# Optimization experiments

Hardware: AMD Instinct MI355X
Metric: run time of the kernel (lower is better)

## Reference

```python
import jax, jax.numpy as jnp
import numpy as np
from jax import lax

B, T = 16384, 10
H = 256
CAR_V, REG_V, POI_V, WEEK_V, TIME_V = 1000000, 100000, 1000, 7, 1440
LABELS = 500
IN = 39  # 16+8+4+3+8


def _lstm_layer(x, Wih, Whh, bih, bhh):
    # x: [B, T, D] -> outputs [B, T, H]; PyTorch gate order i,f,g,o
    b = x.shape[0]
    h0 = jnp.zeros((b, H), x.dtype)
    c0 = jnp.zeros((b, H), x.dtype)
    # Precompute input projections for all timesteps in one GEMM
    xg = jnp.einsum('btd,gd->btg', x, Wih) + bih + bhh  # [B, T, 4H]

    def step(carry, xt_g):
        h, c = carry
        gates = xt_g + h @ Whh.T  # [B, 4H]
        i, f, g, o = jnp.split(gates, 4, axis=-1)
        i, f, o = jax.nn.sigmoid(i), jax.nn.sigmoid(f), jax.nn.sigmoid(o)
        g = jnp.tanh(g)
        c = f * c + i * g
        h = o * jnp.tanh(c)
        return (h, c), h

    _, ys = lax.scan(step, (h0, c0), xg.transpose(1, 0, 2))  # ys: [T, B, H]
    return ys.transpose(1, 0, 2)


def setup_inputs() -> dict:
    key = jax.random.key(0)
    ks = jax.random.split(key, 20)
    s = 0.05
    return {
        'car_idx': jax.random.randint(ks[0], (B, T), 0, CAR_V),
        'region_idx': jax.random.randint(ks[1], (B, T), 0, REG_V),
        'poi_idx': jax.random.randint(ks[2], (B, T), 0, POI_V),
        'week_idx': jax.random.randint(ks[3], (B, T), 0, WEEK_V),
        'time_idx': jax.random.randint(ks[4], (B, T), 0, TIME_V),
        'car_emb': jax.random.normal(ks[5], (CAR_V, 16), jnp.float32) * s,
        'region_emb': jax.random.normal(ks[6], (REG_V, 8), jnp.float32) * s,
        'poi_emb': jax.random.normal(ks[7], (POI_V, 4), jnp.float32) * s,
        'week_emb': jax.random.normal(ks[8], (WEEK_V, 3), jnp.float32) * s,
        'time_emb': jax.random.normal(ks[9], (TIME_V, 8), jnp.float32) * s,
        'Wih0': jax.random.normal(ks[10], (4 * H, IN), jnp.float32) * s,
        'Whh0': jax.random.normal(ks[11], (4 * H, H), jnp.float32) * s,
        'bih0': jax.random.normal(ks[12], (4 * H,), jnp.float32) * s,
        'bhh0': jax.random.normal(ks[13], (4 * H,), jnp.float32) * s,
        'Wih1': jax.random.normal(ks[14], (4 * H, H), jnp.float32) * s,
        'Whh1': jax.random.normal(ks[15], (4 * H, H), jnp.float32) * s,
        'bih1': jax.random.normal(ks[16], (4 * H,), jnp.float32) * s,
        'bhh1': jax.random.normal(ks[17], (4 * H,), jnp.float32) * s,
        'Wout': jax.random.normal(ks[18], (LABELS, H), jnp.float32) * s,
        'bout': jax.random.normal(ks[19], (LABELS,), jnp.float32) * s,
    }


def reference(car_idx, region_idx, poi_idx, week_idx, time_idx,
              car_emb, region_emb, poi_emb, week_emb, time_emb,
              Wih0, Whh0, bih0, bhh0, Wih1, Whh1, bih1, bhh1,
              Wout, bout):
    # Batched version of the original per-item embedding-lookup + concat loop
    x = jnp.concatenate([
        car_emb[car_idx],      # [B, T, 16]
        region_emb[region_idx],  # [B, T, 8]
        poi_emb[poi_idx],      # [B, T, 4]
        week_emb[week_idx],    # [B, T, 3]
        time_emb[time_idx],    # [B, T, 8]
    ], axis=-1)  # [B, T, 39]
    h1 = _lstm_layer(x, Wih0, Whh0, bih0, bhh0)
    h2 = _lstm_layer(h1, Wih1, Whh1, bih1, bhh1)
    return h2[:, -1, :] @ Wout.T + bout  # [B, LABELS]
```

## Files before the change

### kernel.cpp

```cpp
#include <hip/hip_runtime.h>
#include <hip/hip_bf16.h>

#define BB 16384
#define TT 10
#define NLAB 500

typedef __attribute__((ext_vector_type(8))) __bf16 bf16x8;
typedef __attribute__((ext_vector_type(4))) float f32x4;
typedef __attribute__((ext_vector_type(8))) short short8v;

__device__ __forceinline__ unsigned short f2bf(float f) {
  union { float f; unsigned int u; } x; x.f = f;
  unsigned int r = 0x7fffu + ((x.u >> 16) & 1u);
  return (unsigned short)((x.u + r) >> 16);
}

__device__ __forceinline__ float sigm(float x) {
  return __builtin_amdgcn_rcpf(1.f + __builtin_amdgcn_exp2f(-1.4426950408889634f * x));
}
__device__ __forceinline__ float tanh_(float x) {
  float e = __builtin_amdgcn_exp2f(-2.8853900817779268f * x);
  return 2.f * __builtin_amdgcn_rcpf(1.f + e) - 1.f;
}

__device__ __forceinline__ void gload_lds16(const unsigned short* g, unsigned short* l) {
  __builtin_amdgcn_global_load_lds(
      (const __attribute__((address_space(1))) unsigned int*)g,
      (__attribute__((address_space(3))) unsigned int*)l, 16, 0, 0);
}

#define SCHED0() __builtin_amdgcn_sched_barrier(0)
#define BAR_LGKM()                                                       \
  { SCHED0(); asm volatile("s_waitcnt lgkmcnt(0)" ::: "memory");         \
    __builtin_amdgcn_s_barrier(); SCHED0(); }
#define BAR_LGKM_VM4()                                                   \
  { SCHED0(); asm volatile("s_waitcnt vmcnt(4) lgkmcnt(0)" ::: "memory");\
    __builtin_amdgcn_s_barrier(); SCHED0(); }

__global__ void prep_w(const float* __restrict__ Wih0, const float* __restrict__ Whh0,
                       const float* __restrict__ bih0, const float* __restrict__ bhh0,
                       const float* __restrict__ Wih1, const float* __restrict__ Whh1,
                       const float* __restrict__ bih1, const float* __restrict__ bhh1,
                       const float* __restrict__ Wout, const float* __restrict__ bout,
                       unsigned short* __restrict__ wall, float* __restrict__ bblob) {
  int i = blockIdx.x * 256 + threadIdx.x;
  if (i < 983040) {
    int c = i >> 14, r = i & 16383;
    int wid = r >> 11, frag = (r >> 9) & 3, lane = (r >> 3) & 63, e = r & 7;
    int kin = ((lane >> 4) << 3) + e;
    float v;
    if (c < 20) {
      int pass = c / 10, ks = c % 10;
      int n = (pass * 2 + (frag >> 1)) * 256 + wid * 32 + (frag & 1) * 16 + (lane & 15);
      int k = ks * 32 + kin;
      if (k < 64) v = (k < 39) ? Wih0[n * 39 + k] : 0.f;
      else        v = Whh0[n * 256 + (k - 64)];
    } else if (c < 52) {
      int idx = c - 20;
      int pass = idx >> 4, half = (idx >> 3) & 1, ks = idx & 7;
      int n = (pass * 2 + (frag >> 1)) * 256 + wid * 32 + (frag & 1) * 16 + (lane & 15);
      int k = ks * 32 + kin;
      v = half ? Wih1[n * 256 + k]
               : Whh1[n * 256 + k];
    } else {
      int ks = c - 52;
      int n = wid * 64 + frag * 16 + (lane & 15);
      int k = ks * 32 + kin;
      v = (n < NLAB) ? Wout[n * 256 + k] : 0.f;
    }
    wall[i] = f2bf(v);
  } else {
    int j = i - 983040;
    if (j < 1024)       bblob[j] = bih0[j] + bhh0[j];
    else if (j < 2048)  bblob[j] = bih1[j - 1024] + bhh1[j - 1024];
    else if (j < 2560) { int n = j - 2048; bblob[j] = (n < NLAB) ? bout[n] : 0.f; }
  }
}

__global__ void gather_x(const int* __restrict__ car_idx, const int* __restrict__ region_idx,
                         const int* __restrict__ poi_idx, const int* __restrict__ week_idx,
                         const int* __restrict__ time_idx,
                         const float* __restrict__ car_emb, const float* __restrict__ region_emb,
                         const float* __restrict__ poi_emb, const float* __restrict__ week_emb,
                         const float* __restrict__ time_emb,
                         unsigned short* __restrict__ xfrag) {
  int tid = blockIdx.x * 256 + threadIdx.x;
  if (tid >= BB * TT) return;
  int t = tid / BB;
  int b = tid - t * BB;
  int ii = b * TT + t;
  float v[64];
#pragma unroll
  for (int k = 0; k < 64; ++k) v[k] = 0.f;
  { const float* p = car_emb + (size_t)car_idx[ii] * 16;
#pragma unroll
    for (int k = 0; k < 16; ++k) v[k] = p[k]; }
  { const float* p = region_emb + (size_t)region_idx[ii] * 8;
#pragma unroll
    for (int k = 0; k < 8; ++k) v[16 + k] = p[k]; }
  { const float* p = poi_emb + (size_t)poi_idx[ii] * 4;
#pragma unroll
    for (int k = 0; k < 4; ++k) v[24 + k] = p[k]; }
  { const float* p = week_emb + (size_t)week_idx[ii] * 3;
#pragma unroll
    for (int k = 0; k < 3; ++k) v[28 + k] = p[k]; }
  { const float* p = time_emb + (size_t)time_idx[ii] * 8;
#pragma unroll
    for (int k = 0; k < 8; ++k) v[31 + k] = p[k]; }

  int tile = b >> 6, rb = (b >> 4) & 3, lrow = b & 15;
  size_t base = ((size_t)tile * TT + t) * 4096;
#pragma unroll
  for (int c = 0; c < 8; ++c) {
    int kc = c >> 2;
    int lane = lrow + ((c & 3) << 4);
    size_t off = base + (size_t)((((kc << 2) + rb) << 6) + lane) * 8;
    short8v s;
#pragma unroll
    for (int e = 0; e < 8; ++e) s[e] = (short)f2bf(v[c * 8 + e]);
    *(short8v*)(xfrag + off) = s;
  }
}

__device__ __forceinline__ f32x4 MF(bf16x8 a, bf16x8 b, f32x4 c) {
  return __builtin_amdgcn_mfma_f32_16x16x32_bf16(a, b, c, 0, 0, 0);
}

template <int NKS, int SPLIT>
__device__ __forceinline__ void gemm_pass(f32x4 (&acc)[2][2][4], bf16x8 (&bc)[4],
    const unsigned short* wpBase, const unsigned short* wnextFirst,
    const unsigned short* ab1, const unsigned short* ab2, int R0, int lane) {
#define AADDR(J) \
  ((SPLIT < NKS && (J) >= SPLIT) ? (ab2 + ((J) - SPLIT) * 2048) : (ab1 + (J) * 2048))
#define MFMA16(AREG, BREG)                                              \
  { __builtin_amdgcn_s_setprio(1);                                     \
    _Pragma("unroll")                                                   \
    for (int gl = 0; gl < 2; ++gl)                                      \
      _Pragma("unroll")                                                 \
      for (int nb = 0; nb < 2; ++nb)                                    \
        _Pragma("unroll")                                               \
        for (int rb = 0; rb < 4; ++rb)                                  \
          acc[gl][nb][rb] = MF(AREG[rb], BREG[gl * 2 + nb], acc[gl][nb][rb]); \
    __builtin_amdgcn_s_setprio(0); }

  int j = R0;
  bf16x8 aA[4], aB[4];
  {
    const unsigned short* ap = AADDR(j);
#pragma unroll
    for (int rb = 0; rb < 4; ++rb) aA[rb] = *(const bf16x8*)(ap + rb * 512 + lane * 8);
  }
#pragma unroll 1
  for (int i = 0; i < NKS; i += 2) {
    int j1 = j + 1; if (j1 == NKS) j1 = 0;
    bf16x8 bn[4];
    const unsigned short* w1 = wpBase + (size_t)j1 * 16384;
#pragma unroll
    for (int f = 0; f < 4; ++f) bn[f] = *(const bf16x8*)(w1 + f * 512);
    const unsigned short* an = AADDR(j1);
#pragma unroll
    for (int rb = 0; rb < 4; ++rb) aB[rb] = *(const bf16x8*)(an + rb * 512 + lane * 8);
    MFMA16(aA, bc)
    int j2 = j1 + 1; if (j2 == NKS) j2 = 0;
    const unsigned short* w2 = (i + 2 < NKS) ? (wpBase + (size_t)j2 * 16384) : wnextFirst;
#pragma unroll
    for (int f = 0; f < 4; ++f) bc[f] = *(const bf16x8*)(w2 + f * 512);
    const unsigned short* an2 = AADDR((i + 2 < NKS) ? j2 : j1);
#pragma unroll
    for (int rb = 0; rb < 4; ++rb) aA[rb] = *(const bf16x8*)(an2 + rb * 512 + lane * 8);
    MFMA16(aB, bn)
    j = j2;
  }
#undef MFMA16
#undef AADDR
}

__device__ __forceinline__ void partial_if(f32x4 (&acc)[2][2][4], f32x4 (&cst)[2][4],
                                           float* sib) {
#pragma unroll
  for (int nb = 0; nb < 2; ++nb)
#pragma unroll
    for (int rb = 0; rb < 4; ++rb)
#pragma unroll
      for (int r = 0; r < 4; ++r) {
        sib[((nb << 4) + (rb << 2) + r) << 6] = sigm(acc[0][nb][rb][r]);
        cst[nb][rb][r] = sigm(acc[1][nb][rb][r]) * cst[nb][rb][r];
      }
}

__device__ __forceinline__ void finish_go(f32x4 (&acc)[2][2][4], f32x4 (&cst)[2][4],
    const float* sib, unsigned short* hbuf, int lane, int wid) {
  int lrow = ((lane >> 4) << 2);
  int l15 = lane & 15;
#pragma unroll
  for (int nb = 0; nb < 2; ++nb) {
    int jw = (nb << 4) + l15;
    int lane_dst_base = ((jw >> 3) << 4);
    int elem = jw & 7;
#pragma unroll
    for (int rb = 0; rb < 4; ++rb)
#pragma unroll
      for (int r = 0; r < 4; ++r) {
        float g = tanh_(acc[0][nb][rb][r]);
        float o = sigm(acc[1][nb][rb][r]);
        float c = cst[nb][rb][r] + sib[((nb << 4) + (rb << 2) + r) << 6] * g;
        cst[nb][rb][r] = c;
        float h = o * tanh_(c);
        int lane_dst = lrow + r + lane_dst_base;
        hbuf[(size_t)((((wid << 2) + rb) << 6) + lane_dst) * 8 + elem] = f2bf(h);
      }
  }
}

__global__ __launch_bounds__(512, 1) void lstm_fused(
    const unsigned short* __restrict__ xfrag, const unsigned short* __restrict__ wall,
    const float* __restrict__ bblob, float* __restrict__ out) {
  __shared__ __align__(16) unsigned short h1s[16384];
  __shared__ __align__(16) unsigned short h2s[16384];
  __shared__ __align__(16) unsigned short xts[4096];
  __shared__ __align__(16) float bls[2560];
  __shared__ __align__(16) float sis[16384];

  int tid = threadIdx.x, lane = tid & 63, wid = tid >> 6;
  int tile = blockIdx.x, b0 = tile << 6, l15 = lane & 15;

  int R = (tile >> 3) & 15;
  int r2 = R & 1, r8 = R & 7, r16 = R;
  int r10 = (R < 10) ? R : (R - 10);

  for (int i = tid; i < 2560; i += 512) bls[i] = bblob[i];
  gload_lds16(xfrag + (size_t)(tile * TT) * 4096 + wid * 512 + lane * 8, xts + wid * 512);

  float* sib = sis + (wid << 11) + lane;

  const unsigned short* wb = wall + wid * 2048 + lane * 8;

  bf16x8 bc[4];
  {
    const unsigned short* b0p = wb + (size_t)r2 * 16384;
#pragma unroll
    for (int f = 0; f < 4; ++f) bc[f] = *(const bf16x8*)(b0p + f * 512);
  }

  asm volatile("s_waitcnt vmcnt(0)" ::: "memory");
  __syncthreads();

  f32x4 c1[2][4], c2[2][4];
#pragma unroll
  for (int nb = 0; nb < 2; ++nb)
#pragma unroll
    for (int rb = 0; rb < 4; ++rb) {
      c1[nb][rb] = (f32x4){0.f, 0.f, 0.f, 0.f};
      c2[nb][rb] = (f32x4){0.f, 0.f, 0.f, 0.f};
    }
  f32x4 acc[2][2][4];

#define ACC_BIAS(BOFF, GBASE)                                                     \
  _Pragma("unroll")                                                               \
  for (int gl = 0; gl < 2; ++gl)                                                  \
    _Pragma("unroll")                                                             \
    for (int nb = 0; nb < 2; ++nb) {                                              \
      float bv = bls[(BOFF) + (((GBASE) + gl) << 8) + (wid << 5) + (nb << 4) + l15]; \
      _Pragma("unroll")                                                           \
      for (int rb = 0; rb < 4; ++rb) acc[gl][nb][rb] = (f32x4){bv, bv, bv, bv};   \
    }

  ACC_BIAS(0, 0)
  gemm_pass<2, 2>(acc, bc, wb, wb + 163840 + (size_t)r2 * 16384, xts, xts, r2, lane);
  partial_if(acc, c1, sib);
  ACC_BIAS(0, 2)
  gemm_pass<2, 2>(acc, bc, wb + 163840, wb + 458752 + (size_t)r8 * 16384, xts, xts, r2, lane);
  BAR_LGKM()
  gload_lds16(xfrag + (size_t)(tile * TT + 1) * 4096 + wid * 512 + lane * 8,
              xts + wid * 512);
  finish_go(acc, c1, sib, h1s, lane, wid);
  ACC_BIAS(1024, 0)
  BAR_LGKM()
  gemm_pass<8, 8>(acc, bc, wb + 458752, wb + 720896 + (size_t)r8 * 16384, h1s, h1s, r8, lane);
  partial_if(acc, c2, sib);
  ACC_BIAS(1024, 2)
  gemm_pass<8, 8>(acc, bc, wb + 720896, wb + (size_t)r10 * 16384, h1s, h1s, r8, lane);
  BAR_LGKM_VM4()
  finish_go(acc, c2, sib, h2s, lane, wid);

#pragma unroll 1
  for (int t = 1; t < TT; ++t) {
    ACC_BIAS(0, 0)
    gemm_pass<10, 2>(acc, bc, wb, wb + 163840 + (size_t)r10 * 16384, xts, h1s, r10, lane);
    partial_if(acc, c1, sib);
    ACC_BIAS(0, 2)
    gemm_pass<10, 2>(acc, bc, wb + 163840, wb + 327680 + (size_t)r8 * 16384, xts, h1s, r10, lane);
    BAR_LGKM()
    if (t < TT - 1)
      gload_lds16(xfrag + (size_t)(tile * TT + t + 1) * 4096 + wid * 512 + lane * 8,
                  xts + wid * 512);
    finish_go(acc, c1, sib, h1s, lane, wid);
    ACC_BIAS(1024, 0)
    gemm_pass<8, 8>(acc, bc, wb + 327680, wb + 458752 + (size_t)r8 * 16384, h2s, h2s, r8, lane);
    BAR_LGKM()
    gemm_pass<8, 8>(acc, bc, wb + 458752, wb + 589824 + (size_t)r16 * 16384, h1s, h1s, r8, lane);
    partial_if(acc, c2, sib);
    ACC_BIAS(1024, 2)
    gemm_pass<16, 8>(acc, bc, wb + 589824,
                     (t < TT - 1) ? (wb + (size_t)r10 * 16384)
                                  : (wb + 851968 + (size_t)r8 * 16384),
                     h2s, h1s, r16, lane);
    BAR_LGKM_VM4()
    finish_go(acc, c2, sib, h2s, lane, wid);
  }
  BAR_LGKM()

#pragma unroll
  for (int gl = 0; gl < 2; ++gl)
#pragma unroll
    for (int nb = 0; nb < 2; ++nb) {
      float bv = bls[2048 + (wid << 6) + ((gl * 2 + nb) << 4) + l15];
#pragma unroll
      for (int rb = 0; rb < 4; ++rb) acc[gl][nb][rb] = (f32x4){bv, bv, bv, bv};
    }
  gemm_pass<8, 8>(acc, bc, wb + 851968, wb + 851968, h2s, h2s, r8, lane);

#pragma unroll
  for (int gl = 0; gl < 2; ++gl)
#pragma unroll
    for (int nb = 0; nb < 2; ++nb) {
      int n = (wid << 6) + ((gl * 2 + nb) << 4) + l15;
      if (n < NLAB) {
#pragma unroll
        for (int rb = 0; rb < 4; ++rb)
#pragma unroll
          for (int r = 0; r < 4; ++r) {
            int row = (rb << 4) + ((lane >> 4) << 2) + r;
            out[(size_t)(b0 + row) * NLAB + n] = acc[gl][nb][rb][r];
          }
      }
    }
#undef ACC_BIAS
}

extern "C" void kernel_launch(void* const* d_in, const int* in_sizes, int n_in,
                              void* d_out, int out_size, void* d_ws, size_t ws_size,
                              hipStream_t stream) {
  const int* car_idx    = (const int*)d_in[0];
  const int* region_idx = (const int*)d_in[1];
  const int* poi_idx    = (const int*)d_in[2];
  const int* week_idx   = (const int*)d_in[3];
  const int* time_idx   = (const int*)d_in[4];
  const float* car_emb    = (const float*)d_in[5];
  const float* region_emb = (const float*)d_in[6];
  const float* poi_emb    = (const float*)d_in[7];
  const float* week_emb   = (const float*)d_in[8];
  const float* time_emb   = (const float*)d_in[9];
  const float* Wih0 = (const float*)d_in[10];
  const float* Whh0 = (const float*)d_in[11];
  const float* bih0 = (const float*)d_in[12];
  const float* bhh0 = (const float*)d_in[13];
  const float* Wih1 = (const float*)d_in[14];
  const float* Whh1 = (const float*)d_in[15];
  const float* bih1 = (const float*)d_in[16];
  const float* bhh1 = (const float*)d_in[17];
  const float* Wout = (const float*)d_in[18];
  const float* bout = (const float*)d_in[19];

  unsigned short* xfrag = (unsigned short*)d_ws;
  unsigned short* wallp = xfrag + 10485760;
  float* bblob = (float*)(wallp + 983040);

  prep_w<<<3850, 256, 0, stream>>>(Wih0, Whh0, bih0, bhh0, Wih1, Whh1, bih1, bhh1,
                                   Wout, bout, wallp, bblob);
  gather_x<<<640, 256, 0, stream>>>(car_idx, region_idx, poi_idx, week_idx, time_idx,
                                    car_emb, region_emb, poi_emb, week_emb, time_emb, xfrag);
  lstm_fused<<<256, 512, 0, stream>>>(xfrag, wallp, bblob, (float*)d_out);
}
```

Baseline: 268.1 us.

## Keep input gate in registers, use uniform weight pointers, drop rotated K order

The sigmoid of the input gate moves out of a 64 KB shared-memory scratch buffer and into registers, which removes LDS stores and loads between the partial and finish phases. Weight base pointers are made wave-uniform with readfirstlane so address arithmetic can sit in scalar registers. The per-tile rotated starting K-slice (which staggered tiles across weight chunks) is replaced by a fixed linear order. The cost is higher VGPR pressure from the extra 32 floats per thread, and all tiles now read the same weight chunks at the same time, which could raise contention in cache or memory channels.

```diff
diff --git a/kernel.cpp b/kernel.cpp
--- a/kernel.cpp
+++ b/kernel.cpp
@@ -27,6 +27,13 @@
   __builtin_amdgcn_global_load_lds(
       (const __attribute__((address_space(1))) unsigned int*)g,
       (__attribute__((address_space(3))) unsigned int*)l, 16, 0, 0);
+}
+
+__device__ __forceinline__ const unsigned short* uptr(const unsigned short* p) {
+  unsigned long long u = (unsigned long long)p;
+  unsigned int lo = __builtin_amdgcn_readfirstlane((unsigned int)u);
+  unsigned int hi = __builtin_amdgcn_readfirstlane((unsigned int)(u >> 32));
+  return (const unsigned short*)((((unsigned long long)hi) << 32) | lo);
 }
 
 #define SCHED0() __builtin_amdgcn_sched_barrier(0)
@@ -128,10 +135,10 @@
 
 template <int NKS, int SPLIT>
 __device__ __forceinline__ void gemm_pass(f32x4 (&acc)[2][2][4], bf16x8 (&bc)[4],
-    const unsigned short* wpBase, const unsigned short* wnextFirst,
-    const unsigned short* ab1, const unsigned short* ab2, int R0, int lane) {
-#define AADDR(J) \
-  ((SPLIT < NKS && (J) >= SPLIT) ? (ab2 + ((J) - SPLIT) * 2048) : (ab1 + (J) * 2048))
+    const unsigned short* wpU, const unsigned short* wnextU,
+    const unsigned short* ab1, const unsigned short* ab2, int laneB, int lane) {
+#define AADDR(KS) \
+  ((SPLIT < NKS && (KS) >= SPLIT) ? (ab2 + ((KS) - SPLIT) * 2048) : (ab1 + (KS) * 2048))
 #define MFMA16(AREG, BREG)                                              \
   { __builtin_amdgcn_s_setprio(1);                                     \
     _Pragma("unroll")                                                   \
@@ -143,53 +150,50 @@
           acc[gl][nb][rb] = MF(AREG[rb], BREG[gl * 2 + nb], acc[gl][nb][rb]); \
     __builtin_amdgcn_s_setprio(0); }
 
-  int j = R0;
   bf16x8 aA[4], aB[4];
   {
-    const unsigned short* ap = AADDR(j);
-#pragma unroll
-    for (int rb = 0; rb < 4; ++rb) aA[rb] = *(const bf16x8*)(ap + rb * 512 + lane * 8);
+    const unsigned short* a0 = AADDR(0);
+#pragma unroll
+    for (int rb = 0; rb < 4; ++rb) aA[rb] = *(const bf16x8*)(a0 + rb * 512 + lane * 8);
   }
 #pragma unroll 1
-  for (int i = 0; i < NKS; i += 2) {
-    int j1 = j + 1; if (j1 == NKS) j1 = 0;
+  for (int ks = 0; ks < NKS; ks += 2) {
     bf16x8 bn[4];
-    const unsigned short* w1 = wpBase + (size_t)j1 * 16384;
-#pragma unroll
-    for (int f = 0; f < 4; ++f) bn[f] = *(const bf16x8*)(w1 + f * 512);
-    const unsigned short* an = AADDR(j1);
+    const unsigned short* w1 = wpU + 16384;
+#pragma unroll
+    for (int f = 0; f < 4; ++f) bn[f] = *(const bf16x8*)(w1 + laneB + f * 512);
+    const unsigned short* an = AADDR(ks + 1);
 #pragma unroll
     for (int rb = 0; rb < 4; ++rb) aB[rb] = *(const bf16x8*)(an + rb * 512 + lane * 8);
     MFMA16(aA, bc)
-    int j2 = j1 + 1; if (j2 == NKS) j2 = 0;
-    const unsigned short* w2 = (i + 2 < NKS) ? (wpBase + (size_t)j2 * 16384) : wnextFirst;
-#pragma unroll
-    for (int f = 0; f < 4; ++f) bc[f] = *(const bf16x8*)(w2 + f * 512);
-    const unsigned short* an2 = AADDR((i + 2 < NKS) ? j2 : j1);
+    const unsigned short* w2 = (ks + 2 < NKS) ? (wpU + 32768) : wnextU;
+#pragma unroll
+    for (int f = 0; f < 4; ++f) bc[f] = *(const bf16x8*)(w2 + laneB + f * 512);
+    const unsigned short* an2 = AADDR((ks + 2 < NKS) ? (ks + 2) : (NKS - 1));
 #pragma unroll
     for (int rb = 0; rb < 4; ++rb) aA[rb] = *(const bf16x8*)(an2 + rb * 512 + lane * 8);
     MFMA16(aB, bn)
-    j = j2;
+    wpU += 32768;
   }
 #undef MFMA16
 #undef AADDR
 }
 
 __device__ __forceinline__ void partial_if(f32x4 (&acc)[2][2][4], f32x4 (&cst)[2][4],
-                                           float* sib) {
+                                           f32x4 (&si)[2][4]) {
 #pragma unroll
   for (int nb = 0; nb < 2; ++nb)
 #pragma unroll
     for (int rb = 0; rb < 4; ++rb)
 #pragma unroll
       for (int r = 0; r < 4; ++r) {
-        sib[((nb << 4) + (rb << 2) + r) << 6] = sigm(acc[0][nb][rb][r]);
+        si[nb][rb][r] = sigm(acc[0][nb][rb][r]);
         cst[nb][rb][r] = sigm(acc[1][nb][rb][r]) * cst[nb][rb][r];
       }
 }
 
 __device__ __forceinline__ void finish_go(f32x4 (&acc)[2][2][4], f32x4 (&cst)[2][4],
-    const float* sib, unsigned short* hbuf, int lane, int wid) {
+    f32x4 (&si)[2][4], unsigned short* hbuf, int lane, int wid) {
   int lrow = ((lane >> 4) << 2);
   int l15 = lane & 15;
 #pragma unroll
@@ -203,7 +207,7 @@
       for (int r = 0; r < 4; ++r) {
         float g = tanh_(acc[0][nb][rb][r]);
         float o = sigm(acc[1][nb][rb][r]);
-        float c = cst[nb][rb][r] + sib[((nb << 4) + (rb << 2) + r) << 6] * g;
+        float c = cst[nb][rb][r] + si[nb][rb][r] * g;
         cst[nb][rb][r] = c;
         float h = o * tanh_(c);
         int lane_dst = lrow + r + lane_dst_base;
@@ -219,33 +223,25 @@
   __shared__ __align__(16) unsigned short h2s[16384];
   __shared__ __align__(16) unsigned short xts[4096];
   __shared__ __align__(16) float bls[2560];
-  __shared__ __align__(16) float sis[16384];
 
   int tid = threadIdx.x, lane = tid & 63, wid = tid >> 6;
   int tile = blockIdx.x, b0 = tile << 6, l15 = lane & 15;
 
-  int R = (tile >> 3) & 15;
-  int r2 = R & 1, r8 = R & 7, r16 = R;
-  int r10 = (R < 10) ? R : (R - 10);
-
   for (int i = tid; i < 2560; i += 512) bls[i] = bblob[i];
   gload_lds16(xfrag + (size_t)(tile * TT) * 4096 + wid * 512 + lane * 8, xts + wid * 512);
 
-  float* sib = sis + (wid << 11) + lane;
-
-  const unsigned short* wb = wall + wid * 2048 + lane * 8;
+  int uwid = __builtin_amdgcn_readfirstlane(wid);
+  const unsigned short* wbU = uptr(wall) + uwid * 2048;
+  int laneB = lane * 8;
 
   bf16x8 bc[4];
-  {
-    const unsigned short* b0p = wb + (size_t)r2 * 16384;
-#pragma unroll
-    for (int f = 0; f < 4; ++f) bc[f] = *(const bf16x8*)(b0p + f * 512);
-  }
+#pragma unroll
+  for (int f = 0; f < 4; ++f) bc[f] = *(const bf16x8*)(wbU + laneB + f * 512);
 
   asm volatile("s_waitcnt vmcnt(0)" ::: "memory");
   __syncthreads();
 
-  f32x4 c1[2][4], c2[2][4];
+  f32x4 c1[2][4], c2[2][4], si[2][4];
 #pragma unroll
   for (int nb = 0; nb < 2; ++nb)
 #pragma unroll
@@ -266,47 +262,45 @@
     }
 
   ACC_BIAS(0, 0)
-  gemm_pass<2, 2>(acc, bc, wb, wb + 163840 + (size_t)r2 * 16384, xts, xts, r2, lane);
-  partial_if(acc, c1, sib);
+  gemm_pass<2, 2>(acc, bc, wbU, wbU + 163840, xts, xts, laneB, lane);
+  partial_if(acc, c1, si);
   ACC_BIAS(0, 2)
-  gemm_pass<2, 2>(acc, bc, wb + 163840, wb + 458752 + (size_t)r8 * 16384, xts, xts, r2, lane);
+  gemm_pass<2, 2>(acc, bc, wbU + 163840, wbU + 458752, xts, xts, laneB, lane);
   BAR_LGKM()
   gload_lds16(xfrag + (size_t)(tile * TT + 1) * 4096 + wid * 512 + lane * 8,
               xts + wid * 512);
-  finish_go(acc, c1, sib, h1s, lane, wid);
+  finish_go(acc, c1, si, h1s, lane, wid);
   ACC_BIAS(1024, 0)
   BAR_LGKM()
-  gemm_pass<8, 8>(acc, bc, wb + 458752, wb + 720896 + (size_t)r8 * 16384, h1s, h1s, r8, lane);
-  partial_if(acc, c2, sib);
+  gemm_pass<8, 8>(acc, bc, wbU + 458752, wbU + 720896, h1s, h1s, laneB, lane);
+  partial_if(acc, c2, si);
   ACC_BIAS(1024, 2)
-  gemm_pass<8, 8>(acc, bc, wb + 720896, wb + (size_t)r10 * 16384, h1s, h1s, r8, lane);
+  gemm_pass<8, 8>(acc, bc, wbU + 720896, wbU, h1s, h1s, laneB, lane);
   BAR_LGKM_VM4()
-  finish_go(acc, c2, sib, h2s, lane, wid);
+  finish_go(acc, c2, si, h2s, lane, wid);
 
 #pragma unroll 1
   for (int t = 1; t < TT; ++t) {
     ACC_BIAS(0, 0)
-    gemm_pass<10, 2>(acc, bc, wb, wb + 163840 + (size_t)r10 * 16384, xts, h1s, r10, lane);
-    partial_if(acc, c1, sib);
+    gemm_pass<10, 2>(acc, bc, wbU, wbU + 163840, xts, h1s, laneB, lane);
+    partial_if(acc, c1, si);
     ACC_BIAS(0, 2)
-    gemm_pass<10, 2>(acc, bc, wb + 163840, wb + 327680 + (size_t)r8 * 16384, xts, h1s, r10, lane);
+    gemm_pass<10, 2>(acc, bc, wbU + 163840, wbU + 327680, xts, h1s, laneB, lane);
     BAR_LGKM()
     if (t < TT - 1)
       gload_lds16(xfrag + (size_t)(tile * TT + t + 1) * 4096 + wid * 512 + lane * 8,
                   xts + wid * 512);
-    finish_go(acc, c1, sib, h1s, lane, wid);
+    finish_go(acc, c1, si, h1s, lane, wid);
     ACC_BIAS(1024, 0)
-    gemm_pass<8, 8>(acc, bc, wb + 327680, wb + 458752 + (size_t)r8 * 16384, h2s, h2s, r8, lane);
+    gemm_pass<8, 8>(acc, bc, wbU + 327680, wbU + 458752, h2s, h2s, laneB, lane);
     BAR_LGKM()
-    gemm_pass<8, 8>(acc, bc, wb + 458752, wb + 589824 + (size_t)r16 * 16384, h1s, h1s, r8, lane);
-    partial_if(acc, c2, sib);
+    gemm_pass<8, 8>(acc, bc, wbU + 458752, wbU + 589824, h1s, h1s, laneB, lane);
+    partial_if(acc, c2, si);
     ACC_BIAS(1024, 2)
-    gemm_pass<16, 8>(acc, bc, wb + 589824,
-                     (t < TT - 1) ? (wb + (size_t)r10 * 16384)
-                                  : (wb + 851968 + (size_t)r8 * 16384),
-                     h2s, h1s, r16, lane);
+    gemm_pass<16, 8>(acc, bc, wbU + 589824,
+                     (t < TT - 1) ? wbU : (wbU + 851968), h2s, h1s, laneB, lane);
     BAR_LGKM_VM4()
-    finish_go(acc, c2, sib, h2s, lane, wid);
+    finish_go(acc, c2, si, h2s, lane, wid);
   }
   BAR_LGKM()
 
@@ -318,7 +312,7 @@
 #pragma unroll
       for (int rb = 0; rb < 4; ++rb) acc[gl][nb][rb] = (f32x4){bv, bv, bv, bv};
     }
-  gemm_pass<8, 8>(acc, bc, wb + 851968, wb + 851968, h2s, h2s, r8, lane);
+  gemm_pass<8, 8>(acc, bc, wbU + 851968, wbU + 851968, h2s, h2s, laneB, lane);
 
 #pragma unroll
   for (int gl = 0; gl < 2; ++gl)
```

After: 288.4 us. +7.6%, slower.
